# Kernel optimization log

Measured on AMD Instinct MI355X. Metric: run time of the kernel, lower is better.

The kernel has to match this reference:

```python
import jax, jax.numpy as jnp
import numpy as np


def setup_inputs() -> dict:
    key = jax.random.key(0)
    B, T, H, W = 256, 16, 160, 160
    sms = 2
    N = T * (H // sms) * (W // sms)  # 102400 tokens per sample
    k1, _ = jax.random.split(key)
    soft_scores = jax.random.uniform(k1, (B, N), dtype=jnp.float32)
    image_grid_thw = jnp.tile(jnp.array([T, H, W], dtype=jnp.int64), (B, 1))
    return {
        "soft_scores": soft_scores,
        "image_grid_thw": image_grid_thw,
        "spatial_merge_size": sms,
    }


def reference(soft_scores, image_grid_thw, spatial_merge_size,
              lambda_compact=1.0, lambda_tv=1.0, eps=1e-6):
    if soft_scores.ndim == 3:
        soft_scores = soft_scores[..., 0]
    B = soft_scores.shape[0]
    # Uniform grid across the batch (static shapes) -> vectorize over B.
    thw = np.asarray(image_grid_thw)
    t = int(thw[0, 0])
    h = int(thw[0, 1]) // spatial_merge_size
    w = int(thw[0, 2]) // spatial_merge_size
    n = t * h * w

    # s: [B, t, h, w], clamped at 0 like torch clamp_min(0.0)
    s = jnp.maximum(soft_scores[:, :n].astype(jnp.float32).reshape(B, t, h, w), 0.0)
    tot = jnp.maximum(s.sum(axis=(1, 2, 3), keepdims=True), eps)
    p = s / tot  # per-sample normalized distribution

    yy = jnp.linspace(-1.0, 1.0, h, dtype=jnp.float32).reshape(1, 1, h, 1)
    xx = jnp.linspace(-1.0, 1.0, w, dtype=jnp.float32).reshape(1, 1, 1, w)
    mu_x = (p * xx).sum(axis=(1, 2, 3)).reshape(B, 1, 1, 1)
    mu_y = (p * yy).sum(axis=(1, 2, 3)).reshape(B, 1, 1, 1)
    compact = (p * ((xx - mu_x) ** 2 + (yy - mu_y) ** 2)).sum(axis=(1, 2, 3))  # [B]

    tv = jnp.zeros((B,), dtype=jnp.float32)
    if h > 1:
        tv = tv + jnp.abs(s[:, :, 1:, :] - s[:, :, :-1, :]).mean(axis=(1, 2, 3))
    if w > 1:
        tv = tv + jnp.abs(s[:, :, :, 1:] - s[:, :, :, :-1]).mean(axis=(1, 2, 3))
    if t > 1:
        tv = tv + 0.3 * jnp.abs(s[:, 1:, :, :] - s[:, :-1, :, :]).mean(axis=(1, 2, 3))

    return compact.mean() * lambda_compact + tv.mean() * lambda_tv
```

## Files before the change

kernel.cpp:

```cpp
#include <hip/hip_runtime.h>

#define T_DIM 16
#define H2 80
#define W2 80
#define SLICE (H2 * W2)
#define SAMPLE (T_DIM * SLICE)
#define PARTS 3
#define BLOCK 320

__device__ __forceinline__ float4 relu4(float4 v) {
    v.x = fmaxf(v.x, 0.f); v.y = fmaxf(v.y, 0.f);
    v.z = fmaxf(v.z, 0.f); v.w = fmaxf(v.w, 0.f);
    return v;
}

__global__ __launch_bounds__(BLOCK) void tsr_phase1(const float* __restrict__ scores,
                                                    float* __restrict__ ws) {
    __shared__ float red[(BLOCK / 64) * 7];

    const int blk  = blockIdx.x;
    const int b    = blk / PARTS;
    const int band = blk % PARTS;
    const int tid  = threadIdx.x;
    const int lane = tid & 63;

    const float step = 2.0f / (float)(H2 - 1);
    const float* sampBase = scores + (size_t)b * SAMPLE;

    float s0 = 0.f, sx = 0.f, sy = 0.f, sq = 0.f;
    float tvh = 0.f, tvw = 0.f, tvt = 0.f;

    const int cx = tid % 20;
    const int xb = cx * 4;
    const float xx0 = -1.0f + (float)xb * step;
    const float xx1 = xx0 + step, xx2 = xx1 + step, xx3 = xx2 + step;
    const float xs0 = xx0 * xx0, xs1 = xx1 * xx1;
    const float xs2 = xx2 * xx2, xs3 = xx3 * xx3;

    if (band < 2) {
        const int strip = tid / 20;
        const int y0 = band * 32 + strip * 2;
        const int off0 = y0 * W2 + xb;
        const int off1 = off0 + W2;
        const int offH = off1 + W2;
        const int w0   = (cx < 19) ? off0 + 4 : off0 + 3;
        const int w1   = w0 + W2;

        const float yyA = -1.0f + (float)y0 * step;
        const float yyB = yyA + step;
        const float ysA = yyA * yyA, ysB = yyB * yyB;

        float4 prev0 = make_float4(0.f, 0.f, 0.f, 0.f);
        float4 prev1 = prev0;

#pragma unroll 4
        for (int t = 0; t < T_DIM; ++t) {
            const float* sl = sampBase + (size_t)t * SLICE;
            const float4 v0 = relu4(*(const float4*)(sl + off0));
            const float4 v1 = relu4(*(const float4*)(sl + off1));
            const float4 hN = relu4(*(const float4*)(sl + offH));
            const float wn0 = fmaxf(sl[w0], 0.f);
            const float wn1 = fmaxf(sl[w1], 0.f);

            const float c0 = v0.x + v1.x, c1 = v0.y + v1.y;
            const float c2 = v0.z + v1.z, c3 = v0.w + v1.w;
            const float rs0 = (v0.x + v0.y) + (v0.z + v0.w);
            const float rs1 = (v1.x + v1.y) + (v1.z + v1.w);
            s0 += (c0 + c1) + (c2 + c3);
            sx = fmaf(xx0, c0, sx); sx = fmaf(xx1, c1, sx);
            sx = fmaf(xx2, c2, sx); sx = fmaf(xx3, c3, sx);
            sy = fmaf(yyA, rs0, sy); sy = fmaf(yyB, rs1, sy);
            sq = fmaf(xs0, c0, sq); sq = fmaf(xs1, c1, sq);
            sq = fmaf(xs2, c2, sq); sq = fmaf(xs3, c3, sq);
            sq = fmaf(ysA, rs0, sq); sq = fmaf(ysB, rs1, sq);

            tvw += fabsf(v0.y - v0.x) + fabsf(v0.z - v0.y) + fabsf(v0.w - v0.z)
                 + fabsf(wn0 - v0.w)
                 + fabsf(v1.y - v1.x) + fabsf(v1.z - v1.y) + fabsf(v1.w - v1.z)
                 + fabsf(wn1 - v1.w);

            tvh += fabsf(v1.x - v0.x) + fabsf(v1.y - v0.y) +
                   fabsf(v1.z - v0.z) + fabsf(v1.w - v0.w)
                 + fabsf(hN.x - v1.x) + fabsf(hN.y - v1.y) +
                   fabsf(hN.z - v1.z) + fabsf(hN.w - v1.w);

            if (t > 0) {
                tvt += fabsf(v0.x - prev0.x) + fabsf(v0.y - prev0.y) +
                       fabsf(v0.z - prev0.z) + fabsf(v0.w - prev0.w)
                     + fabsf(v1.x - prev1.x) + fabsf(v1.y - prev1.y) +
                       fabsf(v1.z - prev1.z) + fabsf(v1.w - prev1.w);
            }
            prev0 = v0; prev1 = v1;
        }
    } else {
        const int r = tid / 20;
        const int y = 64 + r;
        const int rowOff = y * W2 + xb;
        const int hOff = (y + 1 < H2) ? rowOff + W2 : rowOff;
        const int wOff = (cx < 19) ? rowOff + 4 : rowOff + 3;

        const float yy = -1.0f + (float)y * step;
        const float yy2 = yy * yy;
        const float cq0 = xs0 + yy2, cq1 = xs1 + yy2;
        const float cq2 = xs2 + yy2, cq3 = xs3 + yy2;

        float4 prev = make_float4(0.f, 0.f, 0.f, 0.f);

#pragma unroll 4
        for (int t = 0; t < T_DIM; ++t) {
            const float* sl = sampBase + (size_t)t * SLICE;
            const float4 v  = relu4(*(const float4*)(sl + rowOff));
            const float4 hN = relu4(*(const float4*)(sl + hOff));
            const float  wN = fmaxf(sl[wOff], 0.f);

            const float rs = (v.x + v.y) + (v.z + v.w);
            s0 += rs;
            sy = fmaf(yy, rs, sy);
            sx = fmaf(xx0, v.x, sx); sx = fmaf(xx1, v.y, sx);
            sx = fmaf(xx2, v.z, sx); sx = fmaf(xx3, v.w, sx);
            sq = fmaf(cq0, v.x, sq); sq = fmaf(cq1, v.y, sq);
            sq = fmaf(cq2, v.z, sq); sq = fmaf(cq3, v.w, sq);

            tvw += fabsf(v.y - v.x) + fabsf(v.z - v.y) + fabsf(v.w - v.z)
                 + fabsf(wN - v.w);
            tvh += fabsf(hN.x - v.x) + fabsf(hN.y - v.y) +
                   fabsf(hN.z - v.z) + fabsf(hN.w - v.w);
            if (t > 0) {
                tvt += fabsf(v.x - prev.x) + fabsf(v.y - prev.y) +
                       fabsf(v.z - prev.z) + fabsf(v.w - prev.w);
            }
            prev = v;
        }
    }

    float acc[7] = {s0, sx, sy, sq, tvh, tvw, tvt};
#pragma unroll
    for (int off = 32; off > 0; off >>= 1) {
#pragma unroll
        for (int i = 0; i < 7; ++i) acc[i] += __shfl_down(acc[i], off);
    }
    const int wave = tid >> 6;
    if (lane == 0) {
#pragma unroll
        for (int i = 0; i < 7; ++i) red[wave * 7 + i] = acc[i];
    }
    __syncthreads();
    if (tid < 7) {
        float s = 0.f;
#pragma unroll
        for (int wv = 0; wv < BLOCK / 64; ++wv) s += red[wv * 7 + tid];
        ws[blk * 8 + tid] = s;
    }
}

__global__ __launch_bounds__(256) void tsr_finalize(const float* __restrict__ ws,
                                                    float* __restrict__ out, int B) {
    __shared__ float red[256];
    const int tid = threadIdx.x;
    float acc = 0.f;
    const float ch = 1.0f / (float)(T_DIM * (H2 - 1) * W2);
    const float cw = 1.0f / (float)(T_DIM * H2 * (W2 - 1));
    const float ct = 0.3f / (float)((T_DIM - 1) * H2 * W2);
    for (int b = tid; b < B; b += 256) {
        float p[7] = {0.f, 0.f, 0.f, 0.f, 0.f, 0.f, 0.f};
        for (int part = 0; part < PARTS; ++part) {
            const float* w = ws + (size_t)(b * PARTS + part) * 8;
#pragma unroll
            for (int i = 0; i < 7; ++i) p[i] += w[i];
        }
        const float S0 = p[0], Sx = p[1], Sy = p[2], Sq = p[3];
        const float Th = p[4], Tw = p[5], Tt = p[6];
        const float tot = fmaxf(S0, 1e-6f);
        const float inv = 1.0f / tot;
        const float mux = Sx * inv, muy = Sy * inv;
        const float m2 = mux * mux + muy * muy;
        const float compact = Sq * inv - 2.0f * m2 + m2 * (S0 * inv);
        const float tv = Th * ch + Tw * cw + Tt * ct;
        acc += compact + tv;
    }
    red[tid] = acc;
    __syncthreads();
    for (int s = 128; s > 0; s >>= 1) {
        if (tid < s) red[tid] += red[tid + s];
        __syncthreads();
    }
    if (tid == 0) out[0] = red[0] / (float)B;
}

extern "C" void kernel_launch(void* const* d_in, const int* in_sizes, int n_in,
                              void* d_out, int out_size, void* d_ws, size_t ws_size,
                              hipStream_t stream) {
    const float* scores = (const float*)d_in[0];
    const int B = in_sizes[0] / SAMPLE;
    float* ws = (float*)d_ws;

    tsr_phase1<<<B * PARTS, BLOCK, 0, stream>>>(scores, ws);
    tsr_finalize<<<1, 256, 0, stream>>>(ws, (float*)d_out, B);
}
```

Before: 157.3 us.

## Process four rows per thread and split each sample into two blocks

Each sample is now split across two blocks instead of three. Threads in the first band handle strips of four rows rather than two, covering rows 0-63 in one block. This cuts the redundant halo row load per row pair and reduces block count, in exchange for more registers per thread and fewer blocks overall (512 vs 768). The second band, covering rows 64-79, is unchanged.

Measured after the change: 161.8 us. 2.9% more time.

```diff
diff --git a/kernel.cpp b/kernel.cpp
--- a/kernel.cpp
+++ b/kernel.cpp
@@ -5,7 +5,7 @@
 #define W2 80
 #define SLICE (H2 * W2)
 #define SAMPLE (T_DIM * SLICE)
-#define PARTS 3
+#define PARTS 2
 #define BLOCK 320
 
 __device__ __forceinline__ float4 relu4(float4 v) {
@@ -37,60 +37,62 @@
     const float xs0 = xx0 * xx0, xs1 = xx1 * xx1;
     const float xs2 = xx2 * xx2, xs3 = xx3 * xx3;
 
-    if (band < 2) {
+    if (band == 0) {
         const int strip = tid / 20;
-        const int y0 = band * 32 + strip * 2;
+        const int y0 = strip * 4;
         const int off0 = y0 * W2 + xb;
-        const int off1 = off0 + W2;
-        const int offH = off1 + W2;
+        const int offH = off0 + 4 * W2;
         const int w0   = (cx < 19) ? off0 + 4 : off0 + 3;
-        const int w1   = w0 + W2;
-
-        const float yyA = -1.0f + (float)y0 * step;
-        const float yyB = yyA + step;
-        const float ysA = yyA * yyA, ysB = yyB * yyB;
-
-        float4 prev0 = make_float4(0.f, 0.f, 0.f, 0.f);
-        float4 prev1 = prev0;
-
-#pragma unroll 4
+
+        float yyv[4], ysv[4];
+#pragma unroll
+        for (int k = 0; k < 4; ++k) {
+            yyv[k] = -1.0f + (float)(y0 + k) * step;
+            ysv[k] = yyv[k] * yyv[k];
+        }
+
+        float4 prev[4];
+#pragma unroll
+        for (int k = 0; k < 4; ++k) prev[k] = make_float4(0.f, 0.f, 0.f, 0.f);
+
+#pragma unroll 2
         for (int t = 0; t < T_DIM; ++t) {
             const float* sl = sampBase + (size_t)t * SLICE;
-            const float4 v0 = relu4(*(const float4*)(sl + off0));
-            const float4 v1 = relu4(*(const float4*)(sl + off1));
+            float4 v[4];
+#pragma unroll
+            for (int k = 0; k < 4; ++k)
+                v[k] = relu4(*(const float4*)(sl + off0 + k * W2));
             const float4 hN = relu4(*(const float4*)(sl + offH));
-            const float wn0 = fmaxf(sl[w0], 0.f);
-            const float wn1 = fmaxf(sl[w1], 0.f);
-
-            const float c0 = v0.x + v1.x, c1 = v0.y + v1.y;
-            const float c2 = v0.z + v1.z, c3 = v0.w + v1.w;
-            const float rs0 = (v0.x + v0.y) + (v0.z + v0.w);
-            const float rs1 = (v1.x + v1.y) + (v1.z + v1.w);
+            float wn[4];
+#pragma unroll
+            for (int k = 0; k < 4; ++k)
+                wn[k] = fmaxf(sl[w0 + k * W2], 0.f);
+
+            const float c0 = (v[0].x + v[1].x) + (v[2].x + v[3].x);
+            const float c1 = (v[0].y + v[1].y) + (v[2].y + v[3].y);
+            const float c2 = (v[0].z + v[1].z) + (v[2].z + v[3].z);
+            const float c3 = (v[0].w + v[1].w) + (v[2].w + v[3].w);
             s0 += (c0 + c1) + (c2 + c3);
             sx = fmaf(xx0, c0, sx); sx = fmaf(xx1, c1, sx);
             sx = fmaf(xx2, c2, sx); sx = fmaf(xx3, c3, sx);
-            sy = fmaf(yyA, rs0, sy); sy = fmaf(yyB, rs1, sy);
             sq = fmaf(xs0, c0, sq); sq = fmaf(xs1, c1, sq);
             sq = fmaf(xs2, c2, sq); sq = fmaf(xs3, c3, sq);
-            sq = fmaf(ysA, rs0, sq); sq = fmaf(ysB, rs1, sq);
-
-            tvw += fabsf(v0.y - v0.x) + fabsf(v0.z - v0.y) + fabsf(v0.w - v0.z)
-                 + fabsf(wn0 - v0.w)
-                 + fabsf(v1.y - v1.x) + fabsf(v1.z - v1.y) + fabsf(v1.w - v1.z)
-                 + fabsf(wn1 - v1.w);
-
-            tvh += fabsf(v1.x - v0.x) + fabsf(v1.y - v0.y) +
-                   fabsf(v1.z - v0.z) + fabsf(v1.w - v0.w)
-                 + fabsf(hN.x - v1.x) + fabsf(hN.y - v1.y) +
-                   fabsf(hN.z - v1.z) + fabsf(hN.w - v1.w);
-
-            if (t > 0) {
-                tvt += fabsf(v0.x - prev0.x) + fabsf(v0.y - prev0.y) +
-                       fabsf(v0.z - prev0.z) + fabsf(v0.w - prev0.w)
-                     + fabsf(v1.x - prev1.x) + fabsf(v1.y - prev1.y) +
-                       fabsf(v1.z - prev1.z) + fabsf(v1.w - prev1.w);
+#pragma unroll
+            for (int k = 0; k < 4; ++k) {
+                const float rs = (v[k].x + v[k].y) + (v[k].z + v[k].w);
+                sy = fmaf(yyv[k], rs, sy);
+                sq = fmaf(ysv[k], rs, sq);
+                tvw += fabsf(v[k].y - v[k].x) + fabsf(v[k].z - v[k].y) +
+                       fabsf(v[k].w - v[k].z) + fabsf(wn[k] - v[k].w);
+                const float4 nk = (k < 3) ? v[k + 1] : hN;
+                tvh += fabsf(nk.x - v[k].x) + fabsf(nk.y - v[k].y) +
+                       fabsf(nk.z - v[k].z) + fabsf(nk.w - v[k].w);
+                if (t > 0) {
+                    tvt += fabsf(v[k].x - prev[k].x) + fabsf(v[k].y - prev[k].y) +
+                           fabsf(v[k].z - prev[k].z) + fabsf(v[k].w - prev[k].w);
+                }
+                prev[k] = v[k];
             }
-            prev0 = v0; prev1 = v1;
         }
     } else {
         const int r = tid / 20;
```
